# Optimization experiments

Hardware: AMD Instinct MI355X
Metric: run time of the kernel (lower is better)

## Reference

```python
import jax, jax.numpy as jnp
import numpy as np

IN_DIM = 256
OUT_DIM = 64   # per-head dim
NUM_HEADS = 8
B = 8
N = 1024


def setup_inputs() -> dict:
    key = jax.random.key(0)
    k_adj, k_h, kq, kk, kv, kbq, kbk, kbv = jax.random.split(key, 8)
    adj_matrix = jax.random.randint(k_adj, (N, N), 0, 2, dtype=jnp.int32)
    h = jax.random.normal(k_h, (B, N, IN_DIM), dtype=jnp.float32)
    s = 1.0 / np.sqrt(IN_DIM)
    Wq = jax.random.normal(kq, (IN_DIM, OUT_DIM * NUM_HEADS), dtype=jnp.float32) * s
    Wk = jax.random.normal(kk, (IN_DIM, OUT_DIM * NUM_HEADS), dtype=jnp.float32) * s
    Wv = jax.random.normal(kv, (IN_DIM, OUT_DIM * NUM_HEADS), dtype=jnp.float32) * s
    bq = jax.random.normal(kbq, (OUT_DIM * NUM_HEADS,), dtype=jnp.float32) * 0.01
    bk = jax.random.normal(kbk, (OUT_DIM * NUM_HEADS,), dtype=jnp.float32) * 0.01
    bv = jax.random.normal(kbv, (OUT_DIM * NUM_HEADS,), dtype=jnp.float32) * 0.01
    return {"adj_matrix": adj_matrix, "h": h, "Wq": Wq, "bq": bq,
            "Wk": Wk, "bk": bk, "Wv": Wv, "bv": bv}


def reference(adj_matrix, h, Wq, bq, Wk, bk, Wv, bv):
    B_, N_, _ = h.shape
    H, D = NUM_HEADS, OUT_DIM
    Qh = (h @ Wq + bq).reshape(B_, N_, H, D)
    Kh = (h @ Wk + bk).reshape(B_, N_, H, D)
    Vh = (h @ Wv + bv).reshape(B_, N_, H, D)
    scores = jnp.einsum('bnhd,bmhd->bhnm', Qh, Kh) / jnp.sqrt(jnp.float32(D))
    # adjacency mask broadcast over batch and heads (neigh_attention=True)
    scores = jnp.where(adj_matrix[None, None, :, :] == 0, -jnp.inf, scores)
    attn = jax.nn.softmax(scores, axis=-1)
    out = jnp.einsum('bhnm,bmhd->bnhd', attn, Vh)
    return out.reshape(B_, N_, H * D)
```

## Files before the change

### kernel.cpp

```cpp
#include <hip/hip_runtime.h>
#include <hip/hip_bf16.h>
#include <math.h>

#define IN_DIM 256
#define HD     512
#define NHEADS 8
#define DH     64
#define NSEQ   1024
#define BATCH  8

#define QSCALE 0.18033688011112042f

typedef unsigned short u16;
typedef unsigned int   u32;
typedef short bf16x8 __attribute__((ext_vector_type(8)));
typedef float f32x4  __attribute__((ext_vector_type(4)));
typedef float f32x16 __attribute__((ext_vector_type(16)));
typedef unsigned int u32x2 __attribute__((ext_vector_type(2)));

#if __has_builtin(__builtin_amdgcn_exp2f)
#define EXP2(x) __builtin_amdgcn_exp2f(x)
#else
#define EXP2(x) __expf(0.69314718056f * (x))
#endif

static __device__ __forceinline__ u16 f2bf(float x) {
    u32 u = __builtin_bit_cast(u32, x);
    u += 0x7FFFu + ((u >> 16) & 1u);
    return (u16)(u >> 16);
}
static __device__ __forceinline__ u32 pk(u16 a, u16 b) {
    return (u32)a | ((u32)b << 16);
}
static __device__ __forceinline__ u32 cvtpk(float a, float b) {
    __hip_bfloat162 t = __float22bfloat162_rn(make_float2(a, b));
    u32 r; __builtin_memcpy(&r, &t, 4);
    return r;
}
static __device__ __forceinline__ f32x16 maskinit(uint4 a, uint4 b) {
    f32x16 c;
    u32 ws[8] = {a.x, a.y, a.z, a.w, b.x, b.y, b.z, b.w};
#pragma unroll
    for (int i = 0; i < 8; ++i) {
        c[2 * i]     = __builtin_bit_cast(float, ws[i] << 16);
        c[2 * i + 1] = __builtin_bit_cast(float, ws[i] & 0xFFFF0000u);
    }
    return c;
}

static __device__ __forceinline__ void pswap(u32 &a, u32 &b) {
#if __has_builtin(__builtin_amdgcn_permlane32_swap)
    u32x2 r = __builtin_amdgcn_permlane32_swap(a, b, false, false);
    a = r.x; b = r.y;
#else
    const bool hi = (threadIdx.x & 32) != 0;
    u32 as = (u32)__shfl_xor((int)a, 32, 64);
    u32 bs = (u32)__shfl_xor((int)b, 32, 64);
    u32 na = hi ? bs : a;
    u32 nb = hi ? b  : as;
    a = na; b = nb;
#endif
}

#define MFMA32(a, b, c) __builtin_amdgcn_mfma_f32_32x32x16_bf16(a, b, c, 0, 0, 0)

static __device__ __forceinline__ float sm_pack_half(const f32x16 st, bf16x8* pb) {
    float p[16];
#pragma unroll
    for (int r = 0; r < 16; ++r) p[r] = EXP2(st[r]);
    float t = (((p[0] + p[1]) + (p[2] + p[3])) + ((p[4] + p[5]) + (p[6] + p[7])))
            + (((p[8] + p[9]) + (p[10] + p[11])) + ((p[12] + p[13]) + (p[14] + p[15])));
    uint4 w0, w1;
    w0.x = cvtpk(p[0], p[1]);   w0.y = cvtpk(p[2], p[3]);
    w0.z = cvtpk(p[4], p[5]);   w0.w = cvtpk(p[6], p[7]);
    w1.x = cvtpk(p[8], p[9]);   w1.y = cvtpk(p[10], p[11]);
    w1.z = cvtpk(p[12], p[13]); w1.w = cvtpk(p[14], p[15]);
    pswap(w0.x, w1.x); pswap(w0.y, w1.y); pswap(w0.z, w1.z); pswap(w0.w, w1.w);
    pb[0] = __builtin_bit_cast(bf16x8, w0);
    pb[1] = __builtin_bit_cast(bf16x8, w1);
    return t;
}

__global__ __launch_bounds__(256)
void wtrans_kernel(const float* __restrict__ Wq, const float* __restrict__ Wk,
                   const float* __restrict__ Wv, u16* __restrict__ Wt)
{
    __shared__ float tile[64 * 65];
    const int bid = blockIdx.x, tid = threadIdx.x;
    const int k0 = (bid & 3) * 64, n0 = ((bid >> 2) & 7) * 64, wsel = bid >> 5;
    const float* W = (wsel == 0) ? Wq : (wsel == 1) ? Wk : Wv;
    u16* Out = Wt + (size_t)wsel * HD * IN_DIM;

    const int r = tid >> 2, c0 = (tid & 3) * 16;
#pragma unroll
    for (int j = 0; j < 16; j += 4) {
        float4 v = *(const float4*)(W + (size_t)(k0 + r) * HD + n0 + c0 + j);
        tile[r * 65 + c0 + j + 0] = v.x; tile[r * 65 + c0 + j + 1] = v.y;
        tile[r * 65 + c0 + j + 2] = v.z; tile[r * 65 + c0 + j + 3] = v.w;
    }
    __syncthreads();
    const int n = tid >> 2, ks = (tid & 3) * 16;
    u16 o[16];
#pragma unroll
    for (int j = 0; j < 16; ++j) o[j] = f2bf(tile[(ks + j) * 65 + n]);
    uint4 u0, u1;
    u0.x = pk(o[0], o[1]);   u0.y = pk(o[2], o[3]);
    u0.z = pk(o[4], o[5]);   u0.w = pk(o[6], o[7]);
    u1.x = pk(o[8], o[9]);   u1.y = pk(o[10], o[11]);
    u1.z = pk(o[12], o[13]); u1.w = pk(o[14], o[15]);
    u16* dst = Out + (size_t)(n0 + n) * IN_DIM + k0 + ks;
    *(uint4*)(dst) = u0;
    *(uint4*)(dst + 8) = u1;
}

__global__ __launch_bounds__(256, 4)
void gemm_mask_kernel(const float* __restrict__ h, const u16* __restrict__ Wt,
                      const int* __restrict__ adj,
                      const float* __restrict__ bq, const float* __restrict__ bk,
                      const float* __restrict__ bv,
                      u16* __restrict__ Qg, u16* __restrict__ Kg,
                      u16* __restrict__ Vtg, u16* __restrict__ Madd2)
{
    __shared__ u16 pool[64 * 64 + 3 * 64 * 64];
    const int tid = threadIdx.x;

    if (blockIdx.y >= 8) {
        int* tile = (int*)pool;
        const int abid = (blockIdx.y - 8) * 128 + blockIdx.x;
        const int tR = abid >> 4, tC = abid & 15;
        const int r = tid >> 2, cg = (tid & 3) * 16;
        const int* src = adj + (size_t)(tR * 64 + r) * NSEQ + tC * 64 + cg;
#pragma unroll
        for (int j = 0; j < 16; j += 4) {
            int4 a = *(const int4*)(src + j);
            tile[r * 65 + cg + j + 0] = a.x; tile[r * 65 + cg + j + 1] = a.y;
            tile[r * 65 + cg + j + 2] = a.z; tile[r * 65 + cg + j + 3] = a.w;
        }
        __syncthreads();
        const int q = tid >> 2, p0 = (tid & 3) * 16;
        u16 o[16];
#pragma unroll
        for (int j = 0; j < 16; ++j) {
            const int p = p0 + j;
            const int c = 32 * (p >> 5) + (p & 3) + 4 * ((p >> 4) & 1) + 8 * ((p >> 2) & 3);
            o[j] = (tile[q * 65 + c] == 0) ? (u16)0xFF7F : (u16)0;
        }
        uint4 u0, u1;
        u0.x = pk(o[0], o[1]);   u0.y = pk(o[2], o[3]);
        u0.z = pk(o[4], o[5]);   u0.w = pk(o[6], o[7]);
        u1.x = pk(o[8], o[9]);   u1.y = pk(o[10], o[11]);
        u1.z = pk(o[12], o[13]); u1.w = pk(o[14], o[15]);
        u16* dst = Madd2 + (size_t)(tR * 64 + q) * NSEQ + tC * 64 + p0;
        *(uint4*)(dst) = u0;
        *(uint4*)(dst + 8) = u1;
        return;
    }

    u16* As = pool;
    u16* Bs = pool + 64 * 64;

    const int m0 = blockIdx.x * 64;
    const int hh = blockIdx.y;
    const int n0 = hh * 64;

    const int w = tid >> 6, lane = tid & 63;
    const int l31 = lane & 31, half = lane >> 5;
    const int mh = w & 1, nh = w >> 1;
    const int s7 = l31 & 7;

    f32x16 acc[3] = {};

    const int arw = tid >> 2, acg = (tid & 3) * 2;
    const int brw = tid & 63, bgrp = tid >> 6;
    const float* srcA = h + (size_t)(m0 + arw) * IN_DIM;

    for (int kk = 0; kk < IN_DIM; kk += 64) {
        __syncthreads();
#pragma unroll
        for (int g = 0; g < 2; ++g) {
            const float* p = srcA + kk + (acg + g) * 8;
            float4 v0 = *(const float4*)(p);
            float4 v1 = *(const float4*)(p + 4);
            uint4 u;
            u.x = cvtpk(v0.x, v0.y); u.y = cvtpk(v0.z, v0.w);
            u.z = cvtpk(v1.x, v1.y); u.w = cvtpk(v1.z, v1.w);
            *(uint4*)&As[arw * 64 + (((acg + g) ^ (arw & 7)) * 8)] = u;
        }
#pragma unroll
        for (int i = 0; i < 6; ++i) {
            const int gc = bgrp * 6 + i;
            const int wh = gc >> 3, c8 = gc & 7;
            *(uint4*)&Bs[wh * 4096 + brw * 64 + ((c8 ^ (brw & 7)) * 8)] =
                *(const uint4*)(Wt + (size_t)wh * HD * IN_DIM +
                                (size_t)(n0 + brw) * IN_DIM + kk + c8 * 8);
        }
        __syncthreads();
        const int arow = (32 * mh + l31) * 64;
        const int brow = (32 * nh + l31) * 64;
#pragma unroll
        for (int s = 0; s < 4; ++s) {
            const int g = ((s * 2 + half) ^ s7) * 8;
            bf16x8 a = *(const bf16x8*)&As[arow + g];
#pragma unroll
            for (int wh = 0; wh < 3; ++wh) {
                bf16x8 b = *(const bf16x8*)&Bs[wh * 4096 + brow + g];
                acc[wh] = __builtin_amdgcn_mfma_f32_32x32x16_bf16(a, b, acc[wh], 0, 0, 0);
            }
        }
    }

    for (int which = 0; which < 2; ++which) {
        u16* T = pool;
        const float* bias = (which == 0) ? bq : bk;
        u16* Out = (which == 0) ? Qg : Kg;
        const float scale = (which == 0) ? QSCALE : 1.0f;
        const float bvv = bias[n0 + 32 * nh + l31];
        __syncthreads();
#pragma unroll
        for (int r = 0; r < 16; ++r) {
            const int row = 32 * mh + 4 * half + (r & 3) + 8 * (r >> 2);
            T[row * 72 + 32 * nh + l31] = f2bf((acc[which][r] + bvv) * scale);
        }
        __syncthreads();
        const int row = tid >> 2, qc = (tid & 3) * 16;
        u16* dst = Out + (size_t)(m0 + row) * HD + n0 + qc;
        const u16* srcT = &T[row * 72 + qc];
        *(uint4*)(dst)     = *(const uint4*)(srcT);
        *(uint4*)(dst + 8) = *(const uint4*)(srcT + 8);
    }

    {
        u16* T = pool;
        const int d = 32 * nh + l31;
        const float bvv = bv[n0 + d];
        __syncthreads();
#pragma unroll
        for (int g = 0; g < 4; ++g) {
            ushort4 o;
            o.x = f2bf(acc[2][4 * g + 0] + bvv);
            o.y = f2bf(acc[2][4 * g + 1] + bvv);
            o.z = f2bf(acc[2][4 * g + 2] + bvv);
            o.w = f2bf(acc[2][4 * g + 3] + bvv);
            *(ushort4*)&T[d * 72 + 32 * mh + 16 * half + 4 * g] = o;
        }
        __syncthreads();
        const int b = m0 >> 10, nloc = m0 & 1023;
        const int dd = tid >> 2, c = (tid & 3) * 16;
        u16* dst = Vtg + ((size_t)(b * NHEADS + hh) * DH + dd) * NSEQ + nloc + c;
        *(uint4*)(dst)     = *(uint4*)&T[dd * 72 + c];
        *(uint4*)(dst + 8) = *(uint4*)&T[dd * 72 + c + 8];
    }
}

__global__ __launch_bounds__(256, 2)
void attn_kernel(const u16* __restrict__ Madd2, const u16* __restrict__ Qg,
                 const u16* __restrict__ Kg, const u16* __restrict__ Vtg,
                 float* __restrict__ out)
{
    __shared__ __align__(16) float4 Oex[2048 + 1984];
    __shared__ float Lex[256];

    const int tid = threadIdx.x;
    const int w = tid >> 6, lane = tid & 63;
    const int team = w >> 1, wq = w & 1;
    const int l31 = lane & 31, half = lane >> 5;
    const int bh = blockIdx.x, qt = blockIdx.y;
    const int b = bh >> 3;
    const int n0 = qt * 128;
    const size_t rowbase = (size_t)b * NSEQ;
    const int colbase = (bh & 7) * DH;
    const int qA = wq * 64 + l31;
    const int qB = qA + 32;
    const int cbase = team * 8;

    const u16* qga = Qg + (rowbase + n0 + qA) * HD + colbase;
    const u16* qgb = Qg + (rowbase + n0 + qB) * HD + colbase;
    bf16x8 qbA[4], qbB[4];
#pragma unroll
    for (int s = 0; s < 4; ++s) {
        qbA[s] = *(const bf16x8*)(qga + s * 16 + half * 8);
        qbB[s] = *(const bf16x8*)(qgb + s * 16 + half * 8);
    }

    const u16* kb0 = Kg + (rowbase + cbase * 64 + l31) * HD + colbase + half * 8;
    const u16* kb1 = kb0 + 32 * HD;
    const u16* vb0 = Vtg + ((size_t)bh * DH + l31) * NSEQ + cbase * 64 + half * 8;
    const u16* vb1 = vb0 + 32 * NSEQ;
    const u16* mrowA = Madd2 + (size_t)(n0 + qA) * NSEQ + cbase * 64 + half * 16;
    const u16* mrowB = Madd2 + (size_t)(n0 + qB) * NSEQ + cbase * 64 + half * 16;

    uint4 mA0a = *(const uint4*)(mrowA);
    uint4 mA0b = *(const uint4*)(mrowA + 8);
    uint4 mA1a = *(const uint4*)(mrowA + 32);
    uint4 mA1b = *(const uint4*)(mrowA + 40);
    uint4 mB0a = *(const uint4*)(mrowB);
    uint4 mB0b = *(const uint4*)(mrowB + 8);
    uint4 mB1a = *(const uint4*)(mrowB + 32);
    uint4 mB1b = *(const uint4*)(mrowB + 40);

    float lA = 0.f, lB = 0.f;
    f32x16 OA0 = {}, OA1 = {}, OB0 = {}, OB1 = {};

    for (int ch = 0; ch < 8; ++ch) {
        const u16* kr0 = kb0 + (size_t)ch * 64 * HD;
        const u16* kr1 = kb1 + (size_t)ch * 64 * HD;
        const u16* vr0 = vb0 + ch * 64;
        const u16* vr1 = vb1 + ch * 64;

        f32x16 sA0 = maskinit(mA0a, mA0b);
        f32x16 sB0 = maskinit(mB0a, mB0b);
        {
            bf16x8 k0 = *(const bf16x8*)(kr0);
            bf16x8 k1 = *(const bf16x8*)(kr0 + 16);
            bf16x8 k2 = *(const bf16x8*)(kr0 + 32);
            bf16x8 k3 = *(const bf16x8*)(kr0 + 48);
            sA0 = MFMA32(k0, qbA[0], sA0); sB0 = MFMA32(k0, qbB[0], sB0);
            sA0 = MFMA32(k1, qbA[1], sA0); sB0 = MFMA32(k1, qbB[1], sB0);
            sA0 = MFMA32(k2, qbA[2], sA0); sB0 = MFMA32(k2, qbB[2], sB0);
            sA0 = MFMA32(k3, qbA[3], sA0); sB0 = MFMA32(k3, qbB[3], sB0);
        }
        bf16x8 pbA[2], pbB[2];
        lA += sm_pack_half(sA0, pbA);
        lB += sm_pack_half(sB0, pbB);

        f32x16 sA1 = maskinit(mA1a, mA1b);
        f32x16 sB1 = maskinit(mB1a, mB1b);
        if (ch < 7) {
            const u16* ma = mrowA + (ch + 1) * 64;
            const u16* mb = mrowB + (ch + 1) * 64;
            mA0a = *(const uint4*)(ma);      mA0b = *(const uint4*)(ma + 8);
            mA1a = *(const uint4*)(ma + 32); mA1b = *(const uint4*)(ma + 40);
            mB0a = *(const uint4*)(mb);      mB0b = *(const uint4*)(mb + 8);
            mB1a = *(const uint4*)(mb + 32); mB1b = *(const uint4*)(mb + 40);
        }
        {
            bf16x8 k0 = *(const bf16x8*)(kr1);
            bf16x8 k1 = *(const bf16x8*)(kr1 + 16);
            bf16x8 k2 = *(const bf16x8*)(kr1 + 32);
            bf16x8 k3 = *(const bf16x8*)(kr1 + 48);
            sA1 = MFMA32(k0, qbA[0], sA1); sB1 = MFMA32(k0, qbB[0], sB1);
            sA1 = MFMA32(k1, qbA[1], sA1); sB1 = MFMA32(k1, qbB[1], sB1);
            sA1 = MFMA32(k2, qbA[2], sA1); sB1 = MFMA32(k2, qbB[2], sB1);
            sA1 = MFMA32(k3, qbA[3], sA1); sB1 = MFMA32(k3, qbB[3], sB1);
        }

        {
            bf16x8 v00 = *(const bf16x8*)(vr0);
            bf16x8 v10 = *(const bf16x8*)(vr1);
            bf16x8 v01 = *(const bf16x8*)(vr0 + 16);
            bf16x8 v11 = *(const bf16x8*)(vr1 + 16);
            OA0 = MFMA32(v00, pbA[0], OA0); OA1 = MFMA32(v10, pbA[0], OA1);
            OB0 = MFMA32(v00, pbB[0], OB0); OB1 = MFMA32(v10, pbB[0], OB1);
            OA0 = MFMA32(v01, pbA[1], OA0); OA1 = MFMA32(v11, pbA[1], OA1);
            OB0 = MFMA32(v01, pbB[1], OB0); OB1 = MFMA32(v11, pbB[1], OB1);
        }

        lA += sm_pack_half(sA1, pbA);
        lB += sm_pack_half(sB1, pbB);
        {
            bf16x8 v00 = *(const bf16x8*)(vr0 + 32);
            bf16x8 v10 = *(const bf16x8*)(vr1 + 32);
            bf16x8 v01 = *(const bf16x8*)(vr0 + 48);
            bf16x8 v11 = *(const bf16x8*)(vr1 + 48);
            OA0 = MFMA32(v00, pbA[0], OA0); OA1 = MFMA32(v10, pbA[0], OA1);
            OB0 = MFMA32(v00, pbB[0], OB0); OB1 = MFMA32(v10, pbB[0], OB1);
            OA0 = MFMA32(v01, pbA[1], OA0); OA1 = MFMA32(v11, pbA[1], OA1);
            OB0 = MFMA32(v01, pbB[1], OB0); OB1 = MFMA32(v11, pbB[1], OB1);
        }
    }

    if (team == 1) {
        const int base = wq * 16;
#pragma unroll
        for (int g = 0; g < 4; ++g) {
            float4 t;
            t.x = OA0[4 * g + 0]; t.y = OA0[4 * g + 1];
            t.z = OA0[4 * g + 2]; t.w = OA0[4 * g + 3];
            Oex[(base + g) * 64 + lane] = t;
            t.x = OA1[4 * g + 0]; t.y = OA1[4 * g + 1];
            t.z = OA1[4 * g + 2]; t.w = OA1[4 * g + 3];
            Oex[(base + 4 + g) * 64 + lane] = t;
            t.x = OB0[4 * g + 0]; t.y = OB0[4 * g + 1];
            t.z = OB0[4 * g + 2]; t.w = OB0[4 * g + 3];
            Oex[(base + 8 + g) * 64 + lane] = t;
            t.x = OB1[4 * g + 0]; t.y = OB1[4 * g + 1];
            t.z = OB1[4 * g + 2]; t.w = OB1[4 * g + 3];
            Oex[(base + 12 + g) * 64 + lane] = t;
        }
        Lex[(wq * 2 + 0) * 64 + lane] = lA;
        Lex[(wq * 2 + 1) * 64 + lane] = lB;
    }
    __syncthreads();
    if (team == 0) {
        const int base = wq * 16;
        lA += Lex[(wq * 2 + 0) * 64 + lane];
        lB += Lex[(wq * 2 + 1) * 64 + lane];
#pragma unroll
        for (int g = 0; g < 4; ++g) {
            float4 t0 = Oex[(base + g) * 64 + lane];
            float4 t1 = Oex[(base + 4 + g) * 64 + lane];
            float4 t2 = Oex[(base + 8 + g) * 64 + lane];
            float4 t3 = Oex[(base + 12 + g) * 64 + lane];
            OA0[4 * g + 0] += t0.x; OA0[4 * g + 1] += t0.y;
            OA0[4 * g + 2] += t0.z; OA0[4 * g + 3] += t0.w;
            OA1[4 * g + 0] += t1.x; OA1[4 * g + 1] += t1.y;
            OA1[4 * g + 2] += t1.z; OA1[4 * g + 3] += t1.w;
            OB0[4 * g + 0] += t2.x; OB0[4 * g + 1] += t2.y;
            OB0[4 * g + 2] += t2.z; OB0[4 * g + 3] += t2.w;
            OB1[4 * g + 0] += t3.x; OB1[4 * g + 1] += t3.y;
            OB1[4 * g + 2] += t3.z; OB1[4 * g + 3] += t3.w;
        }

        lA += __shfl_xor(lA, 32, 64);
        lB += __shfl_xor(lB, 32, 64);
        const float invA = 1.0f / lA;
        const float invB = 1.0f / lB;

        float* orowA = out + (rowbase + n0 + qA) * HD + colbase;
        float* orowB = out + (rowbase + n0 + qB) * HD + colbase;
#pragma unroll
        for (int g = 0; g < 4; ++g) {
            const int d0 = 4 * half + 8 * g;
            float4 a0, a1, b0, b1;
            a0.x = OA0[4 * g + 0] * invA; a0.y = OA0[4 * g + 1] * invA;
            a0.z = OA0[4 * g + 2] * invA; a0.w = OA0[4 * g + 3] * invA;
            a1.x = OA1[4 * g + 0] * invA; a1.y = OA1[4 * g + 1] * invA;
            a1.z = OA1[4 * g + 2] * invA; a1.w = OA1[4 * g + 3] * invA;
            b0.x = OB0[4 * g + 0] * invB; b0.y = OB0[4 * g + 1] * invB;
            b0.z = OB0[4 * g + 2] * invB; b0.w = OB0[4 * g + 3] * invB;
            b1.x = OB1[4 * g + 0] * invB; b1.y = OB1[4 * g + 1] * invB;
            b1.z = OB1[4 * g + 2] * invB; b1.w = OB1[4 * g + 3] * invB;
            *(float4*)(orowA + d0)      = a0;
            *(float4*)(orowA + 32 + d0) = a1;
            *(float4*)(orowB + d0)      = b0;
            *(float4*)(orowB + 32 + d0) = b1;
        }
    }
}

extern "C" void kernel_launch(void* const* d_in, const int* in_sizes, int n_in,
                              void* d_out, int out_size, void* d_ws, size_t ws_size,
                              hipStream_t stream) {
    const int*   adj = (const int*)d_in[0];
    const float* h   = (const float*)d_in[1];
    const float* Wq  = (const float*)d_in[2];
    const float* bq  = (const float*)d_in[3];
    const float* Wk  = (const float*)d_in[4];
    const float* bk  = (const float*)d_in[5];
    const float* Wv  = (const float*)d_in[6];
    const float* bv  = (const float*)d_in[7];
    float* outp = (float*)d_out;

    u16* Wt    = (u16*)d_ws;
    u16* Qg    = Wt + (size_t)3 * HD * IN_DIM;
    u16* Kg    = Qg + (size_t)BATCH * NSEQ * HD;
    u16* Vtg   = Kg + (size_t)BATCH * NSEQ * HD;
    u16* Madd2 = Vtg + (size_t)BATCH * NSEQ * HD;
    (void)ws_size;

    wtrans_kernel<<<96, 256, 0, stream>>>(Wq, Wk, Wv, Wt);
    gemm_mask_kernel<<<dim3(BATCH * NSEQ / 64, 10), 256, 0, stream>>>(
        h, Wt, adj, bq, bk, bv, Qg, Kg, Vtg, Madd2);
    attn_kernel<<<dim3(BATCH * NHEADS, NSEQ / 128), 256, 0, stream>>>(
        Madd2, Qg, Kg, Vtg, outp);
}
```

Measured before the change: 151.0 us.

## Stage K/V tiles through swizzled double-buffered LDS shared by each wave pair

K and V chunks are now loaded cooperatively by the 128 threads of each team into XOR-swizzled, double-buffered shared memory. Each chunk is prefetched into registers two iterations ahead. Previously both waves of a team fetched the same K/V fragments straight from global memory, so this cuts redundant global/L2 traffic and lets loads overlap with MFMA work. In exchange it adds a block-wide barrier per chunk, extra LDS reads and writes, and more live registers. The output exchange buffers are now aliased onto the K/V staging arrays.

```diff
diff --git a/kernel.cpp b/kernel.cpp
--- a/kernel.cpp
+++ b/kernel.cpp
@@ -257,8 +257,8 @@
                  const u16* __restrict__ Kg, const u16* __restrict__ Vtg,
                  float* __restrict__ out)
 {
-    __shared__ __align__(16) float4 Oex[2048 + 1984];
-    __shared__ float Lex[256];
+    __shared__ __align__(16) u16 Ks[4][4096];
+    __shared__ __align__(16) u16 Vs[4][4096];
 
     const int tid = threadIdx.x;
     const int w = tid >> 6, lane = tid & 63;
@@ -269,6 +269,7 @@
     const int n0 = qt * 128;
     const size_t rowbase = (size_t)b * NSEQ;
     const int colbase = (bh & 7) * DH;
+    const int q7 = l31 & 7;
     const int qA = wq * 64 + l31;
     const int qB = qA + 32;
     const int cbase = team * 8;
@@ -282,10 +283,14 @@
         qbB[s] = *(const bf16x8*)(qgb + s * 16 + half * 8);
     }
 
-    const u16* kb0 = Kg + (rowbase + cbase * 64 + l31) * HD + colbase + half * 8;
-    const u16* kb1 = kb0 + 32 * HD;
-    const u16* vb0 = Vtg + ((size_t)bh * DH + l31) * NSEQ + cbase * 64 + half * 8;
-    const u16* vb1 = vb0 + 32 * NSEQ;
+    const int ttid = tid & 127;
+    const int srow = ttid >> 1, cg = (ttid & 1) * 4;
+    const int sw0 = ((cg + 0) ^ (srow & 7)) * 8;
+    const int sw1 = ((cg + 1) ^ (srow & 7)) * 8;
+    const int sw2 = ((cg + 2) ^ (srow & 7)) * 8;
+    const int sw3 = ((cg + 3) ^ (srow & 7)) * 8;
+    const u16* kgp = Kg + (rowbase + cbase * 64 + srow) * HD + colbase + cg * 8;
+    const u16* vgp = Vtg + ((size_t)bh * DH + srow) * NSEQ + cbase * 64 + cg * 8;
     const u16* mrowA = Madd2 + (size_t)(n0 + qA) * NSEQ + cbase * 64 + half * 16;
     const u16* mrowB = Madd2 + (size_t)(n0 + qB) * NSEQ + cbase * 64 + half * 16;
 
@@ -298,26 +303,45 @@
     uint4 mB1a = *(const uint4*)(mrowB + 32);
     uint4 mB1b = *(const uint4*)(mrowB + 40);
 
+    uint4 kq0, kq1, kq2, kq3, vq0, vq1, vq2, vq3;
+    kq0 = *(const uint4*)(kgp);      kq1 = *(const uint4*)(kgp + 8);
+    kq2 = *(const uint4*)(kgp + 16); kq3 = *(const uint4*)(kgp + 24);
+    vq0 = *(const uint4*)(vgp);      vq1 = *(const uint4*)(vgp + 8);
+    vq2 = *(const uint4*)(vgp + 16); vq3 = *(const uint4*)(vgp + 24);
+    {
+        u16* kd = &Ks[team * 2][srow * 64];
+        u16* vd = &Vs[team * 2][srow * 64];
+        *(uint4*)&kd[sw0] = kq0; *(uint4*)&kd[sw1] = kq1;
+        *(uint4*)&kd[sw2] = kq2; *(uint4*)&kd[sw3] = kq3;
+        *(uint4*)&vd[sw0] = vq0; *(uint4*)&vd[sw1] = vq1;
+        *(uint4*)&vd[sw2] = vq2; *(uint4*)&vd[sw3] = vq3;
+    }
+    {
+        const u16* kp = kgp + (size_t)64 * HD;
+        const u16* vp = vgp + 64;
+        kq0 = *(const uint4*)(kp);      kq1 = *(const uint4*)(kp + 8);
+        kq2 = *(const uint4*)(kp + 16); kq3 = *(const uint4*)(kp + 24);
+        vq0 = *(const uint4*)(vp);      vq1 = *(const uint4*)(vp + 8);
+        vq2 = *(const uint4*)(vp + 16); vq3 = *(const uint4*)(vp + 24);
+    }
+    __syncthreads();
+
     float lA = 0.f, lB = 0.f;
     f32x16 OA0 = {}, OA1 = {}, OB0 = {}, OB1 = {};
 
     for (int ch = 0; ch < 8; ++ch) {
-        const u16* kr0 = kb0 + (size_t)ch * 64 * HD;
-        const u16* kr1 = kb1 + (size_t)ch * 64 * HD;
-        const u16* vr0 = vb0 + ch * 64;
-        const u16* vr1 = vb1 + ch * 64;
+        const int cur = ch & 1;
+        const u16* Kc = &Ks[team * 2 + cur][0];
+        const u16* Vc = &Vs[team * 2 + cur][0];
 
         f32x16 sA0 = maskinit(mA0a, mA0b);
         f32x16 sB0 = maskinit(mB0a, mB0b);
-        {
-            bf16x8 k0 = *(const bf16x8*)(kr0);
-            bf16x8 k1 = *(const bf16x8*)(kr0 + 16);
-            bf16x8 k2 = *(const bf16x8*)(kr0 + 32);
-            bf16x8 k3 = *(const bf16x8*)(kr0 + 48);
-            sA0 = MFMA32(k0, qbA[0], sA0); sB0 = MFMA32(k0, qbB[0], sB0);
-            sA0 = MFMA32(k1, qbA[1], sA0); sB0 = MFMA32(k1, qbB[1], sB0);
-            sA0 = MFMA32(k2, qbA[2], sA0); sB0 = MFMA32(k2, qbB[2], sB0);
-            sA0 = MFMA32(k3, qbA[3], sA0); sB0 = MFMA32(k3, qbB[3], sB0);
+#pragma unroll
+        for (int s = 0; s < 4; ++s) {
+            const int g = ((s * 2 + half) ^ q7) * 8;
+            bf16x8 ka = *(const bf16x8*)&Kc[l31 * 64 + g];
+            sA0 = MFMA32(ka, qbA[s], sA0);
+            sB0 = MFMA32(ka, qbB[s], sB0);
         }
         bf16x8 pbA[2], pbB[2];
         lA += sm_pack_half(sA0, pbA);
@@ -333,41 +357,55 @@
             mB0a = *(const uint4*)(mb);      mB0b = *(const uint4*)(mb + 8);
             mB1a = *(const uint4*)(mb + 32); mB1b = *(const uint4*)(mb + 40);
         }
-        {
-            bf16x8 k0 = *(const bf16x8*)(kr1);
-            bf16x8 k1 = *(const bf16x8*)(kr1 + 16);
-            bf16x8 k2 = *(const bf16x8*)(kr1 + 32);
-            bf16x8 k3 = *(const bf16x8*)(kr1 + 48);
-            sA1 = MFMA32(k0, qbA[0], sA1); sB1 = MFMA32(k0, qbB[0], sB1);
-            sA1 = MFMA32(k1, qbA[1], sA1); sB1 = MFMA32(k1, qbB[1], sB1);
-            sA1 = MFMA32(k2, qbA[2], sA1); sB1 = MFMA32(k2, qbB[2], sB1);
-            sA1 = MFMA32(k3, qbA[3], sA1); sB1 = MFMA32(k3, qbB[3], sB1);
-        }
-
-        {
-            bf16x8 v00 = *(const bf16x8*)(vr0);
-            bf16x8 v10 = *(const bf16x8*)(vr1);
-            bf16x8 v01 = *(const bf16x8*)(vr0 + 16);
-            bf16x8 v11 = *(const bf16x8*)(vr1 + 16);
-            OA0 = MFMA32(v00, pbA[0], OA0); OA1 = MFMA32(v10, pbA[0], OA1);
-            OB0 = MFMA32(v00, pbB[0], OB0); OB1 = MFMA32(v10, pbB[0], OB1);
-            OA0 = MFMA32(v01, pbA[1], OA0); OA1 = MFMA32(v11, pbA[1], OA1);
-            OB0 = MFMA32(v01, pbB[1], OB0); OB1 = MFMA32(v11, pbB[1], OB1);
+#pragma unroll
+        for (int s = 0; s < 4; ++s) {
+            const int g = ((s * 2 + half) ^ q7) * 8;
+            bf16x8 ka = *(const bf16x8*)&Kc[(32 + l31) * 64 + g];
+            sA1 = MFMA32(ka, qbA[s], sA1);
+            sB1 = MFMA32(ka, qbB[s], sB1);
+        }
+
+        if (ch < 7) {
+            u16* kd = &Ks[team * 2 + (1 - cur)][srow * 64];
+            u16* vd = &Vs[team * 2 + (1 - cur)][srow * 64];
+            *(uint4*)&kd[sw0] = kq0; *(uint4*)&kd[sw1] = kq1;
+            *(uint4*)&kd[sw2] = kq2; *(uint4*)&kd[sw3] = kq3;
+            *(uint4*)&vd[sw0] = vq0; *(uint4*)&vd[sw1] = vq1;
+            *(uint4*)&vd[sw2] = vq2; *(uint4*)&vd[sw3] = vq3;
+        }
+        if (ch < 6) {
+            const u16* kp = kgp + (size_t)(ch + 2) * 64 * HD;
+            const u16* vp = vgp + (ch + 2) * 64;
+            kq0 = *(const uint4*)(kp);      kq1 = *(const uint4*)(kp + 8);
+            kq2 = *(const uint4*)(kp + 16); kq3 = *(const uint4*)(kp + 24);
+            vq0 = *(const uint4*)(vp);      vq1 = *(const uint4*)(vp + 8);
+            vq2 = *(const uint4*)(vp + 16); vq3 = *(const uint4*)(vp + 24);
+        }
+
+#pragma unroll
+        for (int s = 0; s < 2; ++s) {
+            const int g = ((s * 2 + half) ^ q7) * 8;
+            bf16x8 va0 = *(const bf16x8*)&Vc[l31 * 64 + g];
+            bf16x8 va1 = *(const bf16x8*)&Vc[(32 + l31) * 64 + g];
+            OA0 = MFMA32(va0, pbA[s], OA0); OA1 = MFMA32(va1, pbA[s], OA1);
+            OB0 = MFMA32(va0, pbB[s], OB0); OB1 = MFMA32(va1, pbB[s], OB1);
         }
 
         lA += sm_pack_half(sA1, pbA);
         lB += sm_pack_half(sB1, pbB);
-        {
-            bf16x8 v00 = *(const bf16x8*)(vr0 + 32);
-            bf16x8 v10 = *(const bf16x8*)(vr1 + 32);
-            bf16x8 v01 = *(const bf16x8*)(vr0 + 48);
-            bf16x8 v11 = *(const bf16x8*)(vr1 + 48);
-            OA0 = MFMA32(v00, pbA[0], OA0); OA1 = MFMA32(v10, pbA[0], OA1);
-            OB0 = MFMA32(v00, pbB[0], OB0); OB1 = MFMA32(v10, pbB[0], OB1);
-            OA0 = MFMA32(v01, pbA[1], OA0); OA1 = MFMA32(v11, pbA[1], OA1);
-            OB0 = MFMA32(v01, pbB[1], OB0); OB1 = MFMA32(v11, pbB[1], OB1);
-        }
-    }
+#pragma unroll
+        for (int s = 2; s < 4; ++s) {
+            const int g = ((s * 2 + half) ^ q7) * 8;
+            bf16x8 va0 = *(const bf16x8*)&Vc[l31 * 64 + g];
+            bf16x8 va1 = *(const bf16x8*)&Vc[(32 + l31) * 64 + g];
+            OA0 = MFMA32(va0, pbA[s - 2], OA0); OA1 = MFMA32(va1, pbA[s - 2], OA1);
+            OB0 = MFMA32(va0, pbB[s - 2], OB0); OB1 = MFMA32(va1, pbB[s - 2], OB1);
+        }
+        __syncthreads();
+    }
+
+    float4* Oex = (float4*)&Ks[0][0];
+    float*  Lex = (float*)&Vs[0][0];
 
     if (team == 1) {
         const int base = wq * 16;
```

New measurement: 146.0 us. 1.03x faster.
